# Performance work log

Measured on AMD Instinct MI355X. Metric: run time of the kernel, lower is better.

## Reference

```python
import jax, jax.numpy as jnp
import numpy as np

N = 100000      # nodes
F = 128         # feature dim == LSTM hidden dim (num_inputs)
E = 1600000     # edges (avg degree 16)
KARY = 8        # max neighbors per node fed to the LSTM
NPERMS = 4      # eval-time permutations (self.training == False)
NOUT = 64       # num_outputs


def setup_inputs() -> dict:
    key = jax.random.key(0)
    ks = jax.random.split(key, 8)
    s = 0.05
    node_feat = jax.random.normal(ks[0], (N, F), dtype=jnp.float32)
    adjacency = jax.random.randint(ks[1], (E, 2), 0, N, dtype=jnp.int32)
    # LSTM params, torch gate order (i, f, g, o)
    w_ih = jax.random.normal(ks[2], (4 * F, F), dtype=jnp.float32) * s
    w_hh = jax.random.normal(ks[3], (4 * F, F), dtype=jnp.float32) * s
    b_ih = jax.random.normal(ks[4], (4 * F,), dtype=jnp.float32) * s
    b_hh = jax.random.normal(ks[5], (4 * F,), dtype=jnp.float32) * s
    weight = jax.random.normal(ks[6], (2 * F, NOUT), dtype=jnp.float32) * s
    bias = jax.random.normal(ks[7], (NOUT,), dtype=jnp.float32) * s
    return {"node_feat": node_feat, "adjacency": adjacency, "w_ih": w_ih,
            "w_hh": w_hh, "b_ih": b_ih, "b_hh": b_hh,
            "weight": weight, "bias": bias}


def _padded_neighbors(adjacency, perm_key):
    """Random-sample up to KARY neighbors per node (random order), vectorized.
    Returns padded neighbor indices [N, KARY] (-1 pad) and lengths [N]."""
    src, dst = adjacency[:, 0], adjacency[:, 1]
    e = src.shape[0]
    deg = jax.ops.segment_sum(jnp.ones((e,), jnp.int32), src, num_segments=N)
    offsets = jnp.cumsum(deg) - deg  # start of each node's edge block
    r = jax.random.uniform(perm_key, (e,))
    order = jnp.lexsort((r, src))    # sort by src, random tiebreak -> random perm per node
    s2, d2 = src[order], dst[order]
    rank = jnp.arange(e, dtype=jnp.int32) - offsets[s2]  # position within node's list
    slot = jnp.where(rank < KARY, rank, KARY)            # overflow -> dump column
    padded = jnp.full((N, KARY + 1), -1, jnp.int32)
    padded = padded.at[s2, slot].set(d2)
    return padded[:, :KARY], jnp.minimum(deg, KARY)


def _lstm_cn(feats, lengths, w_ih, w_hh, b_ih, b_hh):
    """Masked LSTM over padded sequences; returns final cell state c_n [N, F]
    (state frozen once t >= length, matching pack_padded_sequence semantics)."""
    n, k, f = feats.shape

    def step(carry, inp):
        h, c = carry
        x, t = inp  # x: [n, f]
        gates = x @ w_ih.T + b_ih + h @ w_hh.T + b_hh  # [n, 4f]
        i, fg, g, o = jnp.split(gates, 4, axis=-1)
        i, fg, o = jax.nn.sigmoid(i), jax.nn.sigmoid(fg), jax.nn.sigmoid(o)
        g = jnp.tanh(g)
        c_new = fg * c + i * g
        h_new = o * jnp.tanh(c_new)
        m = (t < lengths)[:, None]
        return (jnp.where(m, h_new, h), jnp.where(m, c_new, c)), None

    init = (jnp.zeros((n, f), feats.dtype), jnp.zeros((n, f), feats.dtype))
    xs = (jnp.swapaxes(feats, 0, 1), jnp.arange(k, dtype=jnp.int32))
    (_, c), _ = jax.lax.scan(step, init, xs)
    return c


def reference(node_feat, adjacency, w_ih, w_hh, b_ih, b_hh, weight, bias):
    key = jax.random.key(42)
    h_neigh = jnp.zeros_like(node_feat)
    for p in range(NPERMS):  # small fixed count, not a data dim
        idx, lengths = _padded_neighbors(adjacency, jax.random.fold_in(key, p))
        feats = node_feat[jnp.maximum(idx, 0)]  # [N, KARY, F]; padding masked via lengths
        h_neigh = h_neigh + _lstm_cn(feats, lengths, w_ih, w_hh, b_ih, b_hh)
    h_neigh = h_neigh * (1.0 / NPERMS)
    return jax.nn.sigmoid(jnp.concatenate([node_feat, h_neigh], axis=1) @ weight + bias)
```

## Files before the change

kernel.cpp:

```cpp
#include <hip/hip_runtime.h>
#include <stdint.h>

#define N_NODES 100000
#define F 128
#define E_EDGES 1600000
#define KARY 8
#define NPERMS 4
#define NOUT 64

typedef __attribute__((ext_vector_type(8))) short bf16x8;
typedef __attribute__((ext_vector_type(4))) float f32x4;

__device__ __forceinline__ uint32_t rotl32(uint32_t v, int r) {
  return (v << r) | (v >> (32 - r));
}
__device__ __forceinline__ void tf2x32(uint32_t k0, uint32_t k1, uint32_t& x0, uint32_t& x1) {
  uint32_t ks2 = k0 ^ k1 ^ 0x1BD11BDAu;
  x0 += k0; x1 += k1;
  x0 += x1; x1 = rotl32(x1,13); x1 ^= x0;
  x0 += x1; x1 = rotl32(x1,15); x1 ^= x0;
  x0 += x1; x1 = rotl32(x1,26); x1 ^= x0;
  x0 += x1; x1 = rotl32(x1, 6); x1 ^= x0;
  x0 += k1; x1 += ks2 + 1u;
  x0 += x1; x1 = rotl32(x1,17); x1 ^= x0;
  x0 += x1; x1 = rotl32(x1,29); x1 ^= x0;
  x0 += x1; x1 = rotl32(x1,16); x1 ^= x0;
  x0 += x1; x1 = rotl32(x1,24); x1 ^= x0;
  x0 += ks2; x1 += k0 + 2u;
  x0 += x1; x1 = rotl32(x1,13); x1 ^= x0;
  x0 += x1; x1 = rotl32(x1,15); x1 ^= x0;
  x0 += x1; x1 = rotl32(x1,26); x1 ^= x0;
  x0 += x1; x1 = rotl32(x1, 6); x1 ^= x0;
  x0 += k0; x1 += k1 + 3u;
  x0 += x1; x1 = rotl32(x1,17); x1 ^= x0;
  x0 += x1; x1 = rotl32(x1,29); x1 ^= x0;
  x0 += x1; x1 = rotl32(x1,16); x1 ^= x0;
  x0 += x1; x1 = rotl32(x1,24); x1 ^= x0;
  x0 += k1; x1 += ks2 + 4u;
  x0 += x1; x1 = rotl32(x1,13); x1 ^= x0;
  x0 += x1; x1 = rotl32(x1,15); x1 ^= x0;
  x0 += x1; x1 = rotl32(x1,26); x1 ^= x0;
  x0 += x1; x1 = rotl32(x1, 6); x1 ^= x0;
  x0 += ks2; x1 += k0 + 5u;
}

__device__ __forceinline__ unsigned short f2bf(float f) {
  uint32_t u = __float_as_uint(f);
  uint32_t r = (u + 0x7FFFu + ((u >> 16) & 1u)) >> 16;
  return (unsigned short)r;
}
__device__ __forceinline__ float ubf(uint32_t u) { return __uint_as_float(u); }

__device__ __forceinline__ f32x4 exp2v(f32x4 x) {
  f32x4 r;
  r.x = __builtin_amdgcn_exp2f(x.x);
  r.y = __builtin_amdgcn_exp2f(x.y);
  r.z = __builtin_amdgcn_exp2f(x.z);
  r.w = __builtin_amdgcn_exp2f(x.w);
  return r;
}
__device__ __forceinline__ f32x4 rcpv(f32x4 x) {
  f32x4 r;
  r.x = __builtin_amdgcn_rcpf(x.x);
  r.y = __builtin_amdgcn_rcpf(x.y);
  r.z = __builtin_amdgcn_rcpf(x.z);
  r.w = __builtin_amdgcn_rcpf(x.w);
  return r;
}
__device__ __forceinline__ f32x4 sig4(f32x4 x) {
  return rcpv(1.0f + exp2v(x * -1.44269504f));
}
__device__ __forceinline__ f32x4 tanh4(f32x4 x) {
  return 1.0f - 2.0f * rcpv(exp2v(x * 2.88539008f) + 1.0f);
}
__device__ __forceinline__ float sigf(float x) {
  return __builtin_amdgcn_rcpf(1.0f + __builtin_amdgcn_exp2f(x * -1.44269504f));
}

#define HIST_BLK (E_EDGES / 256)

__global__ __launch_bounds__(256) void k_hist_prepw(
    const int2* __restrict__ adj, int* __restrict__ deg,
    const float* __restrict__ w_ih, const float* __restrict__ w_hh,
    const float* __restrict__ b_ih, const float* __restrict__ b_hh,
    const float* __restrict__ weight,
    short* __restrict__ wihb, short* __restrict__ whb,
    short* __restrict__ wobT, float4* __restrict__ bq) {
  int b = blockIdx.x;
  if (b < HIST_BLK) {
    int e = b * 256 + threadIdx.x;
    atomicAdd(&deg[adj[e].x], 1);
  } else {
    int t = (b - HIST_BLK) * 256 + threadIdx.x;
    wihb[t] = (short)f2bf(w_ih[t]);
    whb[t] = (short)f2bf(w_hh[t]);
    if (t < 2 * F * NOUT) {
      int n = t & 63, k = t >> 6;
      wobT[n * 256 + k] = (short)f2bf(weight[k * NOUT + n]);
    }
    if (t < F)
      bq[t] = make_float4(b_ih[t] + b_hh[t], b_ih[F + t] + b_hh[F + t],
                          b_ih[2 * F + t] + b_hh[2 * F + t], b_ih[3 * F + t] + b_hh[3 * F + t]);
  }
}

__global__ __launch_bounds__(1024) void k_scanA(const int* __restrict__ deg,
                                                int* __restrict__ rpart,
                                                int* __restrict__ bsum) {
  __shared__ int s[1024];
  int tid = threadIdx.x;
  int i = blockIdx.x * 1024 + tid;
  int v = (i < N_NODES) ? deg[i] : 0;
  s[tid] = v;
  __syncthreads();
  for (int off = 1; off < 1024; off <<= 1) {
    int t = (tid >= off) ? s[tid - off] : 0;
    __syncthreads();
    s[tid] += t;
    __syncthreads();
  }
  if (i < N_NODES) rpart[i] = s[tid] - v;
  if (tid == 1023) bsum[blockIdx.x] = s[tid];
}

__global__ __launch_bounds__(128) void k_scanB(const int* __restrict__ bsum,
                                               int* __restrict__ boff) {
  __shared__ int s[128];
  int tid = threadIdx.x;
  int v = (tid < 98) ? bsum[tid] : 0;
  s[tid] = v;
  __syncthreads();
  for (int off = 1; off < 128; off <<= 1) {
    int t = (tid >= off) ? s[tid - off] : 0;
    __syncthreads();
    s[tid] += t;
    __syncthreads();
  }
  if (tid < 98) boff[tid] = s[tid] - v;
}

__global__ void k_scatter(const int2* __restrict__ adj, const int* __restrict__ rpart,
                          const int* __restrict__ boff, int* __restrict__ cursor,
                          int2* __restrict__ csr) {
  int e = blockIdx.x * blockDim.x + threadIdx.x;
  if (e < E_EDGES) {
    int2 a = adj[e];
    int pos = rpart[a.x] + boff[a.x >> 10] + atomicAdd(&cursor[a.x], 1);
    csr[pos] = make_int2(a.y, e);
  }
}

#define HS_LD 136
#define SEL_BLK ((N_NODES + 255) / 256)

__global__ __launch_bounds__(256) void k_sel_xg(
    const int2* __restrict__ csr, const int* __restrict__ rpart,
    const int* __restrict__ boff,
    const int* __restrict__ deg, int* __restrict__ sel, int* __restrict__ lens,
    const float* __restrict__ feat, const short* __restrict__ wihb,
    const float4* __restrict__ bq, ushort4* __restrict__ xgq) {
  __shared__ short as_[32 * HS_LD];
  if (blockIdx.x < SEL_BLK) {
    int n = blockIdx.x * 256 + threadIdx.x;
    if (n >= N_NODES) return;
    uint32_t pk0[NPERMS], pk1[NPERMS];
#pragma unroll
    for (int p = 0; p < NPERMS; ++p) {
      uint32_t a = 0u, b = (uint32_t)p;
      tf2x32(0u, 42u, a, b);
      pk0[p] = a; pk1[p] = b;
    }
    int off = rpart[n] + boff[n >> 10], d = deg[n];
    unsigned long long key[NPERMS][KARY];
    int nbr[NPERMS][KARY];
#pragma unroll
    for (int p = 0; p < NPERMS; ++p)
#pragma unroll
      for (int i = 0; i < KARY; ++i) { key[p][i] = ~0ULL; nbr[p][i] = -1; }
    for (int e = 0; e < d; ++e) {
      int2 ent = csr[off + e];
#pragma unroll
      for (int p = 0; p < NPERMS; ++p) {
        uint32_t x0 = 0u, x1 = (uint32_t)ent.y;
        tf2x32(pk0[p], pk1[p], x0, x1);
        uint32_t bits = x0 ^ x1;
        unsigned long long k = ((unsigned long long)(bits >> 9) << 21) | (unsigned)ent.y;
        if (k < key[p][KARY - 1]) {
          key[p][KARY - 1] = k; nbr[p][KARY - 1] = ent.x;
#pragma unroll
          for (int s = KARY - 1; s >= 1; --s) {
            if (key[p][s] < key[p][s - 1]) {
              unsigned long long tk = key[p][s]; key[p][s] = key[p][s - 1]; key[p][s - 1] = tk;
              int tn = nbr[p][s]; nbr[p][s] = nbr[p][s - 1]; nbr[p][s - 1] = tn;
            }
          }
        }
      }
    }
    int L = d < KARY ? d : KARY;
    lens[n] = L;
#pragma unroll
    for (int p = 0; p < NPERMS; ++p)
#pragma unroll
      for (int t = 0; t < KARY; ++t)
        sel[((size_t)p * N_NODES + n) * KARY + t] = (t < L) ? nbr[p][t] : -1;
  } else {
    const int tid = threadIdx.x;
    const int w = tid >> 6, l = tid & 63;
    const int l15 = l & 15, q = l >> 4;
    const int nb = (blockIdx.x - SEL_BLK) * 32;
#pragma unroll
    for (int i = 0; i < 4; ++i) {
      int idx = tid + i * 256;
      int row = idx >> 5, c4 = (idx & 31) * 4;
      float4 v = *(const float4*)&feat[(size_t)(nb + row) * F + c4];
      ushort4 s;
      s.x = f2bf(v.x); s.y = f2bf(v.y); s.z = f2bf(v.z); s.w = f2bf(v.w);
      *(ushort4*)&as_[row * HS_LD + c4] = s;
    }
    __syncthreads();

    f32x4 acc[2][2][4];
#pragma unroll
    for (int mt = 0; mt < 2; ++mt)
#pragma unroll
      for (int ft = 0; ft < 2; ++ft)
#pragma unroll
        for (int g4 = 0; g4 < 4; ++g4) acc[mt][ft][g4] = (f32x4){0.f, 0.f, 0.f, 0.f};

    const short* ab = as_ + l15 * HS_LD + q * 8;
#pragma unroll
    for (int kt = 0; kt < 4; ++kt) {
      bf16x8 a0 = *(const bf16x8*)(ab + kt * 32);
      bf16x8 a1 = *(const bf16x8*)(ab + 16 * HS_LD + kt * 32);
#pragma unroll
      for (int g4 = 0; g4 < 4; ++g4)
#pragma unroll
        for (int ft = 0; ft < 2; ++ft) {
          bf16x8 b = *(const bf16x8*)(wihb + (size_t)(g4 * 128 + 16 * ft + 32 * w + l15) * F + q * 8 + kt * 32);
          acc[0][ft][g4] = __builtin_amdgcn_mfma_f32_16x16x32_bf16(a0, b, acc[0][ft][g4], 0, 0, 0);
          acc[1][ft][g4] = __builtin_amdgcn_mfma_f32_16x16x32_bf16(a1, b, acc[1][ft][g4], 0, 0, 0);
        }
    }
#pragma unroll
    for (int mt = 0; mt < 2; ++mt)
#pragma unroll
      for (int ft = 0; ft < 2; ++ft) {
        int fi = 32 * w + 16 * ft + l15;
        float4 bb = bq[fi];
#pragma unroll
        for (int r = 0; r < 4; ++r) {
          int node = nb + mt * 16 + q * 4 + r;
          ushort4 o;
          o.x = f2bf(acc[mt][ft][0][r] + bb.x);
          o.y = f2bf(acc[mt][ft][1][r] + bb.y);
          o.z = f2bf(acc[mt][ft][2][r] + bb.z);
          o.w = f2bf(acc[mt][ft][3][r] + bb.w);
          xgq[(size_t)node * F + fi] = o;
        }
      }
  }
}

#define LB 8
#define OS_LD 264
__global__ __launch_bounds__(256, 2) void k_lstm(const short* __restrict__ whb,
                                                 const ushort4* __restrict__ xgq,
                                                 const int* __restrict__ sel,
                                                 const int* __restrict__ lens,
                                                 const float* __restrict__ feat,
                                                 const short* __restrict__ wobT,
                                                 const float* __restrict__ bias,
                                                 float* __restrict__ out) {
  __shared__ short hs[32 * HS_LD];
  __shared__ int sel_l[32][9];
  const int tid = threadIdx.x;
  const int w = tid >> 6;
  const int l = tid & 63;
  const int l15 = l & 15, q = l >> 4;
  const int nb = blockIdx.x * LB;
  const char* xgb = (const char*)xgq;
  const int fi8 = (32 * w + l15) * 8;

  {
    int m = tid >> 3, t = tid & 7;
    int node = nb + (m >> 2), p = m & 3;
    sel_l[m][t] = sel[((size_t)p * N_NODES + node) * KARY + t];
  }
  {
    int* h32 = (int*)hs;
    for (int i = tid; i < 32 * HS_LD / 2; i += 256) h32[i] = 0;
  }
  uint32_t lp = 0;
#pragma unroll
  for (int i = 0; i < 8; ++i) lp |= (uint32_t)lens[nb + i] << (4 * i);

  bf16x8 breg[4][4][2];
#pragma unroll
  for (int kt = 0; kt < 4; ++kt)
#pragma unroll
    for (int g4 = 0; g4 < 4; ++g4)
#pragma unroll
      for (int ft = 0; ft < 2; ++ft)
        breg[kt][g4][ft] = *(const bf16x8*)(whb + (size_t)(g4 * 128 + 16 * ft + 32 * w + l15) * F + q * 8 + kt * 32);

  const short* abase = hs + l15 * HS_LD + q * 8;

  f32x4 cst[2][2];
#pragma unroll
  for (int mt = 0; mt < 2; ++mt)
#pragma unroll
    for (int ft = 0; ft < 2; ++ft) cst[mt][ft] = (f32x4){0.f, 0.f, 0.f, 0.f};

  __syncthreads();

  for (int t = 0; t < KARY; ++t) {
    uint2 xr[2][4][2];
#pragma unroll
    for (int mt = 0; mt < 2; ++mt)
#pragma unroll
      for (int r = 0; r < 4; ++r) {
        int seq = mt * 16 + q * 4 + r;
        int v = sel_l[seq][t];
        v = v < 0 ? 0 : v;
        int off = (v << 10) + fi8;
        xr[mt][r][0] = *(const uint2*)(xgb + off);
        xr[mt][r][1] = *(const uint2*)(xgb + off + 128);
      }

    f32x4 acc[2][2][4];
#pragma unroll
    for (int mt = 0; mt < 2; ++mt)
#pragma unroll
      for (int ft = 0; ft < 2; ++ft)
#pragma unroll
        for (int g4 = 0; g4 < 4; ++g4) acc[mt][ft][g4] = (f32x4){0.f, 0.f, 0.f, 0.f};

#pragma unroll
    for (int kt = 0; kt < 4; ++kt) {
      bf16x8 a0 = *(const bf16x8*)(abase + 0 * 16 * HS_LD + kt * 32);
      bf16x8 a1 = *(const bf16x8*)(abase + 1 * 16 * HS_LD + kt * 32);
#pragma unroll
      for (int g4 = 0; g4 < 4; ++g4)
#pragma unroll
        for (int ft = 0; ft < 2; ++ft) {
          acc[0][ft][g4] = __builtin_amdgcn_mfma_f32_16x16x32_bf16(a0, breg[kt][g4][ft], acc[0][ft][g4], 0, 0, 0);
          acc[1][ft][g4] = __builtin_amdgcn_mfma_f32_16x16x32_bf16(a1, breg[kt][g4][ft], acc[1][ft][g4], 0, 0, 0);
        }
    }
    __syncthreads();

#pragma unroll
    for (int mt = 0; mt < 2; ++mt) {
      int len = (lp >> (4 * (mt * 4 + q))) & 15;
      bool live = t < len;
#pragma unroll
      for (int ft = 0; ft < 2; ++ft) {
        f32x4 xi, xf, xg_, xo;
#pragma unroll
        for (int r = 0; r < 4; ++r) {
          uint2 x = xr[mt][r][ft];
          xi[r] = ubf(x.x << 16);
          xf[r] = ubf(x.x & 0xffff0000u);
          xg_[r] = ubf(x.y << 16);
          xo[r] = ubf(x.y & 0xffff0000u);
        }
        f32x4 ii = sig4(acc[mt][ft][0] + xi);
        f32x4 ff = sig4(acc[mt][ft][1] + xf);
        f32x4 gg = tanh4(acc[mt][ft][2] + xg_);
        f32x4 oo = sig4(acc[mt][ft][3] + xo);
        f32x4 cn = ff * cst[mt][ft] + ii * gg;
        if (live) {
          cst[mt][ft] = cn;
          f32x4 hh = oo * tanh4(cn);
          int base = (mt * 16 + q * 4) * HS_LD + 32 * w + 16 * ft + l15;
#pragma unroll
          for (int r = 0; r < 4; ++r)
            hs[base + r * HS_LD] = (short)f2bf(hh[r]);
        }
      }
    }
    __syncthreads();
  }

  short* as2 = hs;

#pragma unroll
  for (int mt = 0; mt < 2; ++mt)
#pragma unroll
    for (int ft = 0; ft < 2; ++ft) {
      f32x4 cc = cst[mt][ft];
      float hv = (cc.x + cc.y + cc.z + cc.w) * 0.25f;
      as2[(mt * 4 + q) * OS_LD + 128 + 32 * w + 16 * ft + l15] = (short)f2bf(hv);
    }
  {
    int row = tid >> 5, c4 = (tid & 31) * 4;
    float4 v = *(const float4*)&feat[(size_t)(nb + row) * F + c4];
    ushort4 s;
    s.x = f2bf(v.x); s.y = f2bf(v.y); s.z = f2bf(v.z); s.w = f2bf(v.w);
    *(ushort4*)&as2[row * OS_LD + c4] = s;
  }
  float bb = bias[16 * w + l15];
  __syncthreads();

  f32x4 oacc = (f32x4){0.f, 0.f, 0.f, 0.f};
  const short* ab2 = as2 + l15 * OS_LD + q * 8;
#pragma unroll
  for (int kt = 0; kt < 8; ++kt) {
    bf16x8 a = *(const bf16x8*)(ab2 + kt * 32);
    bf16x8 b = *(const bf16x8*)(wobT + (size_t)(16 * w + l15) * 256 + q * 8 + kt * 32);
    oacc = __builtin_amdgcn_mfma_f32_16x16x32_bf16(a, b, oacc, 0, 0, 0);
  }
  if (q < 2) {
#pragma unroll
    for (int r = 0; r < 4; ++r) {
      int node = nb + q * 4 + r;
      out[(size_t)node * NOUT + 16 * w + l15] = sigf(oacc[r] + bb);
    }
  }
}

extern "C" void kernel_launch(void* const* d_in, const int* in_sizes, int n_in,
                              void* d_out, int out_size, void* d_ws, size_t ws_size,
                              hipStream_t stream) {
  const float* feat = (const float*)d_in[0];
  const int2* adj = (const int2*)d_in[1];
  const float* w_ih = (const float*)d_in[2];
  const float* w_hh = (const float*)d_in[3];
  const float* b_ih = (const float*)d_in[4];
  const float* b_hh = (const float*)d_in[5];
  const float* weight = (const float*)d_in[6];
  const float* bias = (const float*)d_in[7];
  float* out = (float*)d_out;

  size_t off = 0;
  auto take = [&](size_t bytes) -> void* {
    void* p = (char*)d_ws + off;
    off += (bytes + 255) & ~(size_t)255;
    return p;
  };
  int* deg = (int*)take((size_t)N_NODES * 4);
  int* rpart = (int*)take((size_t)N_NODES * 4);
  int* cursor = (int*)take((size_t)N_NODES * 4);
  int2* csr = (int2*)take((size_t)E_EDGES * 8);
  int* sel = (int*)take((size_t)NPERMS * N_NODES * KARY * 4);
  int* lens = (int*)take((size_t)N_NODES * 4);
  short* wihb = (short*)take((size_t)4 * F * F * 2);
  short* whb = (short*)take((size_t)4 * F * F * 2);
  short* wobT = (short*)take((size_t)NOUT * 2 * F * 2);
  float4* bq = (float4*)take((size_t)F * 16);
  ushort4* xgq = (ushort4*)take((size_t)N_NODES * F * 8);
  int* bsum = (int*)take(128 * 4);
  int* boff = (int*)take(128 * 4);
  (void)ws_size; (void)in_sizes; (void)n_in; (void)out_size;

  hipMemsetAsync(deg, 0, (size_t)N_NODES * 4, stream);
  hipMemsetAsync(cursor, 0, (size_t)N_NODES * 4, stream);

  k_hist_prepw<<<HIST_BLK + 256, 256, 0, stream>>>(adj, deg, w_ih, w_hh, b_ih, b_hh,
                                                   weight, wihb, whb, wobT, bq);
  k_scanA<<<98, 1024, 0, stream>>>(deg, rpart, bsum);
  k_scanB<<<1, 128, 0, stream>>>(bsum, boff);
  k_scatter<<<(E_EDGES + 255) / 256, 256, 0, stream>>>(adj, rpart, boff, cursor, csr);
  k_sel_xg<<<SEL_BLK + N_NODES / 32, 256, 0, stream>>>(csr, rpart, boff, deg, sel, lens,
                                                       feat, wihb, bq, xgq);
  k_lstm<<<N_NODES / LB, 256, 0, stream>>>(whb, xgq, sel, lens, feat, wobT, bias, out);
}
```

Measured before the change: 1.298 ms.

## Double-buffer LSTM hidden state, prescale gate weights, pack bf16 converts

The LSTM hidden state in LDS is now ping-ponged between two buffers. Each recurrence step reads one buffer and writes the other, so one of the two block barriers per timestep can be dropped. The gate weights and biases are pre-multiplied by -log2(e) when they are converted, which removes the per-element scale multiply inside the sigmoid and tanh gate math. The bf16 stores of h now use the packed v_cvt_pk_bf16_f32 instruction in place of manual rounding. The cost is double the LDS used for hidden state, which could affect occupancy, and frozen rows may hold a stale h, which is harmless because only the cell state is used.

```diff
diff --git a/kernel.cpp b/kernel.cpp
--- a/kernel.cpp
+++ b/kernel.cpp
@@ -50,6 +50,11 @@
   return (unsigned short)r;
 }
 __device__ __forceinline__ float ubf(uint32_t u) { return __uint_as_float(u); }
+__device__ __forceinline__ uint32_t cvtpk(float lo, float hi) {
+  uint32_t r;
+  asm("v_cvt_pk_bf16_f32 %0, %1, %2" : "=v"(r) : "v"(lo), "v"(hi));
+  return r;
+}
 
 __device__ __forceinline__ f32x4 exp2v(f32x4 x) {
   f32x4 r;
@@ -67,8 +72,11 @@
   r.w = __builtin_amdgcn_rcpf(x.w);
   return r;
 }
-__device__ __forceinline__ f32x4 sig4(f32x4 x) {
-  return rcpv(1.0f + exp2v(x * -1.44269504f));
+__device__ __forceinline__ f32x4 sig4p(f32x4 y) {
+  return rcpv(1.0f + exp2v(y));
+}
+__device__ __forceinline__ f32x4 tanh4p(f32x4 y) {
+  return 1.0f - 2.0f * rcpv(exp2v(y * -2.0f) + 1.0f);
 }
 __device__ __forceinline__ f32x4 tanh4(f32x4 x) {
   return 1.0f - 2.0f * rcpv(exp2v(x * 2.88539008f) + 1.0f);
@@ -76,6 +84,8 @@
 __device__ __forceinline__ float sigf(float x) {
   return __builtin_amdgcn_rcpf(1.0f + __builtin_amdgcn_exp2f(x * -1.44269504f));
 }
+
+#define GSC -1.44269504f
 
 #define HIST_BLK (E_EDGES / 256)
 
@@ -85,22 +95,23 @@
     const float* __restrict__ b_ih, const float* __restrict__ b_hh,
     const float* __restrict__ weight,
     short* __restrict__ wihb, short* __restrict__ whb,
-    short* __restrict__ wobT, float4* __restrict__ bq) {
+    float4* __restrict__ bq, short* __restrict__ wobT) {
   int b = blockIdx.x;
   if (b < HIST_BLK) {
     int e = b * 256 + threadIdx.x;
     atomicAdd(&deg[adj[e].x], 1);
   } else {
     int t = (b - HIST_BLK) * 256 + threadIdx.x;
-    wihb[t] = (short)f2bf(w_ih[t]);
-    whb[t] = (short)f2bf(w_hh[t]);
+    wihb[t] = (short)f2bf(w_ih[t] * GSC);
+    whb[t] = (short)f2bf(w_hh[t] * GSC);
     if (t < 2 * F * NOUT) {
       int n = t & 63, k = t >> 6;
       wobT[n * 256 + k] = (short)f2bf(weight[k * NOUT + n]);
     }
     if (t < F)
-      bq[t] = make_float4(b_ih[t] + b_hh[t], b_ih[F + t] + b_hh[F + t],
-                          b_ih[2 * F + t] + b_hh[2 * F + t], b_ih[3 * F + t] + b_hh[3 * F + t]);
+      bq[t] = make_float4(GSC * (b_ih[t] + b_hh[t]), GSC * (b_ih[F + t] + b_hh[F + t]),
+                          GSC * (b_ih[2 * F + t] + b_hh[2 * F + t]),
+                          GSC * (b_ih[3 * F + t] + b_hh[3 * F + t]));
   }
 }
 
@@ -272,7 +283,7 @@
                                                  const short* __restrict__ wobT,
                                                  const float* __restrict__ bias,
                                                  float* __restrict__ out) {
-  __shared__ short hs[32 * HS_LD];
+  __shared__ short hs[2][32 * HS_LD];
   __shared__ int sel_l[32][9];
   const int tid = threadIdx.x;
   const int w = tid >> 6;
@@ -289,7 +300,7 @@
   }
   {
     int* h32 = (int*)hs;
-    for (int i = tid; i < 32 * HS_LD / 2; i += 256) h32[i] = 0;
+    for (int i = tid; i < 32 * HS_LD; i += 256) h32[i] = 0;
   }
   uint32_t lp = 0;
 #pragma unroll
@@ -304,7 +315,8 @@
       for (int ft = 0; ft < 2; ++ft)
         breg[kt][g4][ft] = *(const bf16x8*)(whb + (size_t)(g4 * 128 + 16 * ft + 32 * w + l15) * F + q * 8 + kt * 32);
 
-  const short* abase = hs + l15 * HS_LD + q * 8;
+  const short* ab0 = hs[0] + l15 * HS_LD + q * 8;
+  const short* ab1 = hs[1] + l15 * HS_LD + q * 8;
 
   f32x4 cst[2][2];
 #pragma unroll
@@ -314,7 +326,7 @@
 
   __syncthreads();
 
-  for (int t = 0; t < KARY; ++t) {
+  auto lstm_step = [&](int t, const short* abase, short* hw) {
     uint2 xr[2][4][2];
 #pragma unroll
     for (int mt = 0; mt < 2; ++mt)
@@ -348,7 +360,6 @@
           acc[1][ft][g4] = __builtin_amdgcn_mfma_f32_16x16x32_bf16(a1, breg[kt][g4][ft], acc[1][ft][g4], 0, 0, 0);
         }
     }
-    __syncthreads();
 
 #pragma unroll
     for (int mt = 0; mt < 2; ++mt) {
@@ -365,25 +376,33 @@
           xg_[r] = ubf(x.y << 16);
           xo[r] = ubf(x.y & 0xffff0000u);
         }
-        f32x4 ii = sig4(acc[mt][ft][0] + xi);
-        f32x4 ff = sig4(acc[mt][ft][1] + xf);
-        f32x4 gg = tanh4(acc[mt][ft][2] + xg_);
-        f32x4 oo = sig4(acc[mt][ft][3] + xo);
+        f32x4 ii = sig4p(acc[mt][ft][0] + xi);
+        f32x4 ff = sig4p(acc[mt][ft][1] + xf);
+        f32x4 gg = tanh4p(acc[mt][ft][2] + xg_);
+        f32x4 oo = sig4p(acc[mt][ft][3] + xo);
         f32x4 cn = ff * cst[mt][ft] + ii * gg;
         if (live) {
           cst[mt][ft] = cn;
           f32x4 hh = oo * tanh4(cn);
           int base = (mt * 16 + q * 4) * HS_LD + 32 * w + 16 * ft + l15;
-#pragma unroll
-          for (int r = 0; r < 4; ++r)
-            hs[base + r * HS_LD] = (short)f2bf(hh[r]);
+          uint32_t p01 = cvtpk(hh[0], hh[1]);
+          uint32_t p23 = cvtpk(hh[2], hh[3]);
+          hw[base + 0 * HS_LD] = (short)p01;
+          hw[base + 1 * HS_LD] = (short)(p01 >> 16);
+          hw[base + 2 * HS_LD] = (short)p23;
+          hw[base + 3 * HS_LD] = (short)(p23 >> 16);
         }
       }
     }
     __syncthreads();
-  }
-
-  short* as2 = hs;
+  };
+
+  for (int tt = 0; tt < KARY; tt += 2) {
+    lstm_step(tt, ab0, hs[1]);
+    lstm_step(tt + 1, ab1, hs[0]);
+  }
+
+  short* as2 = hs[0];
 
 #pragma unroll
   for (int mt = 0; mt < 2; ++mt)
@@ -458,7 +477,7 @@
   hipMemsetAsync(cursor, 0, (size_t)N_NODES * 4, stream);
 
   k_hist_prepw<<<HIST_BLK + 256, 256, 0, stream>>>(adj, deg, w_ih, w_hh, b_ih, b_hh,
-                                                   weight, wihb, whb, wobT, bq);
+                                                   weight, wihb, whb, bq, wobT);
   k_scanA<<<98, 1024, 0, stream>>>(deg, rpart, bsum);
   k_scanB<<<1, 128, 0, stream>>>(bsum, boff);
   k_scatter<<<(E_EDGES + 255) / 256, 256, 0, stream>>>(adj, rpart, boff, cursor, csr);
```

Measured after the change: 1.275 ms. About the same (-1.8%).
